# Kernel optimization log

Hardware: AMD Instinct MI355X
Metric: run time of the kernel (lower is better)

## Reference

```python
import jax, jax.numpy as jnp
import numpy as np

N = 50000
D = 128           # feature_dim
H = 8             # num_heads
DH = D // H       # head_dim = 16
K = 32            # k_neighbors
FFN = int(D * 1.5)  # 192
TAU_NEG = 0.6
BETA = 1.5
LN_EPS = 1e-5


def layer_norm(x, g, b):
    mu = jnp.mean(x, axis=-1, keepdims=True)
    var = jnp.mean((x - mu) ** 2, axis=-1, keepdims=True)
    return (x - mu) * jax.lax.rsqrt(var + LN_EPS) * g + b


def setup_inputs() -> dict:
    key = jax.random.key(0)
    ks = jax.random.split(key, 12)
    s = 1.0 / np.sqrt(D)
    inp = {
        "features": jax.random.normal(ks[0], (N, D), dtype=jnp.float32),
        "knn_indices": jax.random.randint(ks[1], (N, K), 0, N, dtype=jnp.int64 if jax.config.jax_enable_x64 else jnp.int32),
        "spatial_distances": jax.random.uniform(ks[2], (N, K), dtype=jnp.float32) * 8.0,
        "Wq": jax.random.normal(ks[3], (D, D), dtype=jnp.float32) * s,
        "Wk": jax.random.normal(ks[4], (D, D), dtype=jnp.float32) * s,
        "Wv": jax.random.normal(ks[5], (D, D), dtype=jnp.float32) * s,
        "Wo": jax.random.normal(ks[6], (D, D), dtype=jnp.float32) * s,
        "bo": jnp.zeros((D,), dtype=jnp.float32),
        "ln1_g": jnp.ones((D,), dtype=jnp.float32),
        "ln1_b": jnp.zeros((D,), dtype=jnp.float32),
        "W1": jax.random.normal(ks[7], (D, FFN), dtype=jnp.float32) * s,
        "b1": jnp.zeros((FFN,), dtype=jnp.float32),
        "W2": jax.random.normal(ks[8], (FFN, D), dtype=jnp.float32) * (1.0 / np.sqrt(FFN)),
        "b2": jnp.zeros((D,), dtype=jnp.float32),
        "ln2_g": jnp.ones((D,), dtype=jnp.float32),
        "ln2_b": jnp.zeros((D,), dtype=jnp.float32),
    }
    return inp


def reference(features, knn_indices, spatial_distances, Wq, Wk, Wv, Wo, bo,
              ln1_g, ln1_b, W1, b1, W2, b2, ln2_g, ln2_b):
    n = features.shape[0]
    Q = (features @ Wq).reshape(n, H, DH)           # (N,H,dh)
    Kp = (features @ Wk).reshape(n, H, DH)
    Vp = (features @ Wv).reshape(n, H, DH)

    K_local = Kp[knn_indices]                        # (N,K,H,dh) irregular gather
    V_local = Vp[knn_indices]                        # (N,K,H,dh)

    raw_scores = jnp.einsum("nhd,nkhd->nhk", Q, K_local) / np.sqrt(DH)  # (N,H,K)

    # per-head spatial decay: 1 / 2^(h+1)
    head_scalings = (0.5 ** jnp.arange(1, H + 1, dtype=features.dtype))  # (H,)
    scaled_dist = spatial_distances[:, None, :] * head_scalings[None, :, None]  # (N,H,K)

    attn_pos = jax.nn.softmax(raw_scores - scaled_dist, axis=-1)
    attn_neg = jax.nn.softmax((-raw_scores - scaled_dist) / TAU_NEG, axis=-1)
    attn = attn_pos - BETA * attn_neg                # (N,H,K); dropout is identity in eval

    attended = jnp.einsum("nhk,nkhd->nhd", attn, V_local).reshape(n, D)

    x = attended @ Wo + bo + features
    x = layer_norm(x, ln1_g, ln1_b)

    h = jax.nn.gelu(x @ W1 + b1, approximate=False)
    ffn_out = h @ W2 + b2
    out = layer_norm(ffn_out + x, ln2_g, ln2_b)
    return out
```

## Files before the change

### kernel.cpp

```cpp
#include <hip/hip_runtime.h>
#include <hip/hip_fp16.h>
#include <cmath>

typedef __attribute__((ext_vector_type(8))) _Float16 f16x8;
typedef __attribute__((ext_vector_type(4))) float f32x4;

__device__ __forceinline__ unsigned int pkh(float a, float b) {
    __half2 h = __floats2half2_rn(a, b);
    return *(unsigned int*)&h;
}
__device__ __forceinline__ float gelu_exact(float v) {
    return 0.5f * v * (1.0f + erff(v * 0.70710678118654752440f));
}
__device__ __forceinline__ __half2 shfl8h(__half2 x, int m) {
    int xi = *(int*)&x;
    int yi = __shfl_xor(xi, m, 8);
    return *(__half2*)&yi;
}

__global__ __launch_bounds__(256, 1) void k_prep(
    const float* __restrict__ Wq, const float* __restrict__ Wk, const float* __restrict__ Wv,
    const float* __restrict__ Wo, const float* __restrict__ W1, const float* __restrict__ W2,
    unsigned short* __restrict__ wsz)
{
    int f = blockIdx.x * 256 + threadIdx.x;
    const float* W; unsigned short* dst; int M, KS, fl;
    if (f < 2048)       { W = Wq; dst = wsz;         M = 128; KS = 4; fl = f; }
    else if (f < 4096)  { W = Wk; dst = wsz + 16384; M = 128; KS = 4; fl = f - 2048; }
    else if (f < 6144)  { W = Wv; dst = wsz + 32768; M = 128; KS = 4; fl = f - 4096; }
    else if (f < 8192)  { W = Wo; dst = wsz + 49152; M = 128; KS = 4; fl = f - 6144; }
    else if (f < 11264) { W = W1; dst = wsz + 65536; M = 192; KS = 4; fl = f - 8192; }
    else if (f < 14336) { W = W2; dst = wsz + 90112; M = 128; KS = 6; fl = f - 11264; }
    else return;
    const int l  = fl & 63;
    const int ks = (fl >> 6) % KS;
    const int ct = (fl >> 6) / KS;
    const int k0 = ks * 32 + (l >> 4) * 8;
    const int col = ct * 16 + (l & 15);
    unsigned short tmp[8];
    #pragma unroll
    for (int j = 0; j < 8; ++j) {
        __half hh = __float2half(W[(size_t)(k0 + j) * M + col]);
        tmp[j] = *(unsigned short*)&hh;
    }
    ((uint4*)dst)[fl] = *(uint4*)tmp;
}

__global__ __launch_bounds__(256, 4) void k_qkv(
    const float* __restrict__ feat, const unsigned short* __restrict__ wsz,
    unsigned short* __restrict__ Qb, unsigned short* __restrict__ KVb, int n)
{
    const int w = threadIdx.x >> 6, lane = threadIdx.x & 63;
    const int lrow = lane & 15, kgrp = lane >> 4;
    const int node = blockIdx.x * 64 + w * 16 + lrow;
    const bool valid = node < n;

    f16x8 bfr[4];
    #pragma unroll
    for (int ks = 0; ks < 4; ++ks) {
        float4 lo = make_float4(0.f, 0.f, 0.f, 0.f), hi = lo;
        if (valid) {
            const float* p = feat + (size_t)node * 128 + ks * 32 + kgrp * 8;
            lo = *(const float4*)p;
            hi = *(const float4*)(p + 4);
        }
        f16x8 b;
        b[0] = (_Float16)lo.x; b[1] = (_Float16)lo.y; b[2] = (_Float16)lo.z; b[3] = (_Float16)lo.w;
        b[4] = (_Float16)hi.x; b[5] = (_Float16)hi.y; b[6] = (_Float16)hi.z; b[7] = (_Float16)hi.w;
        bfr[ks] = b;
    }

    for (int mat = 0; mat < 3; ++mat) {
        const unsigned short* wb = wsz + mat * 16384;
        f32x4 acc[8];
        #pragma unroll
        for (int ct = 0; ct < 8; ++ct) acc[ct] = (f32x4){0.f, 0.f, 0.f, 0.f};
        #pragma unroll
        for (int ct = 0; ct < 8; ++ct)
            #pragma unroll
            for (int ks = 0; ks < 4; ++ks) {
                f16x8 afr = *(const f16x8*)(wb + ((size_t)(ct * 4 + ks) * 64 + lane) * 8);
                acc[ct] = __builtin_amdgcn_mfma_f32_16x16x32_f16(afr, bfr[ks], acc[ct], 0, 0, 0);
            }
        if (valid) {
            unsigned short* O = (mat == 0) ? (Qb + (size_t)node * 128)
                              : (KVb + (size_t)node * 256 + (mat == 2 ? 128 : 0));
            #pragma unroll
            for (int ct = 0; ct < 8; ++ct) {
                int col = ct * 16 + kgrp * 4;
                *((uint2*)(O + col)) =
                    make_uint2(pkh(acc[ct][0], acc[ct][1]), pkh(acc[ct][2], acc[ct][3]));
            }
        }
    }
}

__global__ __launch_bounds__(256, 4) void k_attn(
    const unsigned short* __restrict__ Qb, const unsigned short* __restrict__ KVb,
    const int* __restrict__ knn, const float* __restrict__ dist,
    unsigned short* __restrict__ attf, int n)
{
    const int lane = threadIdx.x & 63;
    const int node = blockIdx.x * 4 + (threadIdx.x >> 6);
    if (node >= n) return;
    const int h = lane >> 3, r = lane & 7;
    const float hs = exp2f(-(float)(h + 1));

    int idx[4]; float sd[4];
    #pragma unroll
    for (int jj = 0; jj < 4; ++jj) {
        int j = r + jj * 8;
        idx[jj] = knn[(size_t)node * 32 + j];
        sd[jj]  = dist[(size_t)node * 32 + j] * hs;
    }

    const unsigned short* qp = Qb + (size_t)node * 128 + h * 16;
    __half2 q2[8];
    *((uint4*)&q2[0]) = *(const uint4*)qp;
    *((uint4*)&q2[4]) = *(const uint4*)(qp + 8);

    uint4 k0[4], k1[4], v0[4], v1[4];
    #pragma unroll
    for (int jj = 0; jj < 4; ++jj) {
        const unsigned short* kvp = KVb + (size_t)idx[jj] * 256 + h * 16;
        k0[jj] = *(const uint4*)kvp;
        k1[jj] = *(const uint4*)(kvp + 8);
        v0[jj] = *(const uint4*)(kvp + 128);
        v1[jj] = *(const uint4*)(kvp + 136);
    }

    float ap[4], an[4];
    #pragma unroll
    for (int jj = 0; jj < 4; ++jj) {
        const __half2* ka = (const __half2*)&k0[jj];
        const __half2* kb = (const __half2*)&k1[jj];
        __half2 s0 = __hmul2(q2[0], ka[0]);
        s0 = __hfma2(q2[1], ka[1], s0);
        s0 = __hfma2(q2[2], ka[2], s0);
        s0 = __hfma2(q2[3], ka[3], s0);
        __half2 s1 = __hmul2(q2[4], kb[0]);
        s1 = __hfma2(q2[5], kb[1], s1);
        s1 = __hfma2(q2[6], kb[2], s1);
        s1 = __hfma2(q2[7], kb[3], s1);
        float s = __low2float(s0) + __high2float(s0) + __low2float(s1) + __high2float(s1);
        float raw = s * 0.25f;
        ap[jj] = raw - sd[jj];
        an[jj] = (-raw - sd[jj]) * (1.0f / 0.6f);
    }

    float mp = fmaxf(fmaxf(ap[0], ap[1]), fmaxf(ap[2], ap[3]));
    float mn = fmaxf(fmaxf(an[0], an[1]), fmaxf(an[2], an[3]));
    #pragma unroll
    for (int msk = 1; msk < 8; msk <<= 1) {
        mp = fmaxf(mp, __shfl_xor(mp, msk, 8));
        mn = fmaxf(mn, __shfl_xor(mn, msk, 8));
    }
    float ep[4], en[4], sp = 0.f, sn = 0.f;
    #pragma unroll
    for (int jj = 0; jj < 4; ++jj) {
        ep[jj] = expf(ap[jj] - mp); sp += ep[jj];
        en[jj] = expf(an[jj] - mn); sn += en[jj];
    }
    #pragma unroll
    for (int msk = 1; msk < 8; msk <<= 1) {
        sp += __shfl_xor(sp, msk, 8);
        sn += __shfl_xor(sn, msk, 8);
    }
    const float isp = 1.0f / sp;
    const float isn = 1.5f / sn;

    __half2 acc2[8];
    #pragma unroll
    for (int i = 0; i < 8; ++i) acc2[i] = __float2half2_rn(0.f);
    #pragma unroll
    for (int jj = 0; jj < 4; ++jj) {
        float wgt = ep[jj] * isp - en[jj] * isn;
        __half2 w2 = __float2half2_rn(wgt);
        const __half2* va = (const __half2*)&v0[jj];
        const __half2* vb = (const __half2*)&v1[jj];
        acc2[0] = __hfma2(w2, va[0], acc2[0]);
        acc2[1] = __hfma2(w2, va[1], acc2[1]);
        acc2[2] = __hfma2(w2, va[2], acc2[2]);
        acc2[3] = __hfma2(w2, va[3], acc2[3]);
        acc2[4] = __hfma2(w2, vb[0], acc2[4]);
        acc2[5] = __hfma2(w2, vb[1], acc2[5]);
        acc2[6] = __hfma2(w2, vb[2], acc2[6]);
        acc2[7] = __hfma2(w2, vb[3], acc2[7]);
    }
    #pragma unroll
    for (int i = 0; i < 8; ++i) {
        acc2[i] = __hadd2(acc2[i], shfl8h(acc2[i], 1));
        acc2[i] = __hadd2(acc2[i], shfl8h(acc2[i], 2));
        acc2[i] = __hadd2(acc2[i], shfl8h(acc2[i], 4));
    }
    if (r == 0) {
        const int g = node >> 4, lrow = node & 15;
        unsigned short* op = attf + (size_t)g * 2048 + (h >> 1) * 512 + (h & 1) * 256 + lrow * 8;
        *((uint4*)op)         = *(uint4*)&acc2[0];
        *((uint4*)(op + 128)) = *(uint4*)&acc2[4];
    }
}

__global__ __launch_bounds__(256, 4) void k_tail(
    const unsigned short* __restrict__ attf, const float* __restrict__ feat,
    const unsigned short* __restrict__ wsz,
    const float* __restrict__ bo, const float* __restrict__ g1, const float* __restrict__ b1ln,
    const float* __restrict__ b1f, const float* __restrict__ b2f,
    const float* __restrict__ g2, const float* __restrict__ b2ln,
    float* __restrict__ out, int n)
{
    __shared__ __align__(16) unsigned short hls[12288];
    const int tid = threadIdx.x;
    const int w = tid >> 6, lane = tid & 63;
    const int lrow = lane & 15, kgrp = lane >> 4;
    const int node = blockIdx.x * 64 + w * 16 + lrow;
    const bool valid = node < n;
    const int g = blockIdx.x * 4 + w;

    f16x8 bfr[6];
    #pragma unroll
    for (int ks = 0; ks < 4; ++ks) {
        uint4 u = make_uint4(0u, 0u, 0u, 0u);
        if (valid) u = *(const uint4*)(attf + (size_t)g * 2048 + ks * 512 + kgrp * 128 + lrow * 8);
        bfr[ks] = *(f16x8*)&u;
    }
    const unsigned short* wo = wsz + 49152;
    f32x4 X[8];
    #pragma unroll
    for (int ct = 0; ct < 8; ++ct) {
        X[ct] = (f32x4){0.f, 0.f, 0.f, 0.f};
        #pragma unroll
        for (int ks = 0; ks < 4; ++ks) {
            f16x8 afr = *(const f16x8*)(wo + ((size_t)(ct * 4 + ks) * 64 + lane) * 8);
            X[ct] = __builtin_amdgcn_mfma_f32_16x16x32_f16(afr, bfr[ks], X[ct], 0, 0, 0);
        }
    }
    #pragma unroll
    for (int ct = 0; ct < 8; ++ct) {
        int col = ct * 16 + kgrp * 4;
        float4 bv = *((const float4*)(bo + col));
        float4 fr = make_float4(0.f, 0.f, 0.f, 0.f);
        if (valid) fr = *((const float4*)(feat + (size_t)node * 128 + col));
        X[ct][0] += bv.x + fr.x; X[ct][1] += bv.y + fr.y;
        X[ct][2] += bv.z + fr.z; X[ct][3] += bv.w + fr.w;
    }
    float s = 0.f;
    #pragma unroll
    for (int ct = 0; ct < 8; ++ct) s += X[ct][0] + X[ct][1] + X[ct][2] + X[ct][3];
    s += __shfl_xor(s, 16); s += __shfl_xor(s, 32);
    const float mu1 = s * (1.0f / 128.0f);
    float s2 = 0.f;
    #pragma unroll
    for (int ct = 0; ct < 8; ++ct)
        #pragma unroll
        for (int rr = 0; rr < 4; ++rr) { float d = X[ct][rr] - mu1; s2 = fmaf(d, d, s2); }
    s2 += __shfl_xor(s2, 16); s2 += __shfl_xor(s2, 32);
    const float rs1 = rsqrtf(s2 * (1.0f / 128.0f) + 1e-5f);

    uint2 xnh[8];
    #pragma unroll
    for (int ct = 0; ct < 8; ++ct) {
        int col = ct * 16 + kgrp * 4;
        float4 gg = *((const float4*)(g1 + col));
        float4 bb = *((const float4*)(b1ln + col));
        float x0 = (X[ct][0] - mu1) * rs1 * gg.x + bb.x;
        float x1 = (X[ct][1] - mu1) * rs1 * gg.y + bb.y;
        float x2 = (X[ct][2] - mu1) * rs1 * gg.z + bb.z;
        float x3 = (X[ct][3] - mu1) * rs1 * gg.w + bb.w;
        xnh[ct] = make_uint2(pkh(x0, x1), pkh(x2, x3));
        int ks = col >> 5, kg = (col & 31) >> 3, jb = col & 7;
        *((uint2*)&hls[((w * 4 + ks) * 4 + kg) * 128 + lrow * 8 + jb]) = xnh[ct];
    }
    __syncthreads();
    #pragma unroll
    for (int ks = 0; ks < 4; ++ks)
        bfr[ks] = *(const f16x8*)&hls[((w * 4 + ks) * 4 + kgrp) * 128 + lrow * 8];
    __syncthreads();

    const unsigned short* w1 = wsz + 65536;
    #pragma unroll
    for (int ct = 0; ct < 12; ++ct) {
        f32x4 acc = (f32x4){0.f, 0.f, 0.f, 0.f};
        #pragma unroll
        for (int ks = 0; ks < 4; ++ks) {
            f16x8 afr = *(const f16x8*)(w1 + ((size_t)(ct * 4 + ks) * 64 + lane) * 8);
            acc = __builtin_amdgcn_mfma_f32_16x16x32_f16(afr, bfr[ks], acc, 0, 0, 0);
        }
        int col = ct * 16 + kgrp * 4;
        float4 bv = *((const float4*)(b1f + col));
        float h0 = gelu_exact(acc[0] + bv.x);
        float h1 = gelu_exact(acc[1] + bv.y);
        float h2 = gelu_exact(acc[2] + bv.z);
        float h3 = gelu_exact(acc[3] + bv.w);
        int ks = col >> 5, kg = (col & 31) >> 3, jb = col & 7;
        *((uint2*)&hls[((w * 6 + ks) * 4 + kg) * 128 + lrow * 8 + jb]) =
            make_uint2(pkh(h0, h1), pkh(h2, h3));
    }
    __syncthreads();
    #pragma unroll
    for (int ks = 0; ks < 6; ++ks)
        bfr[ks] = *(const f16x8*)&hls[((w * 6 + ks) * 4 + kgrp) * 128 + lrow * 8];

    const unsigned short* w2 = wsz + 90112;
    f32x4 Y[8];
    #pragma unroll
    for (int ct = 0; ct < 8; ++ct) {
        Y[ct] = (f32x4){0.f, 0.f, 0.f, 0.f};
        #pragma unroll
        for (int ks = 0; ks < 6; ++ks) {
            f16x8 afr = *(const f16x8*)(w2 + ((size_t)(ct * 6 + ks) * 64 + lane) * 8);
            Y[ct] = __builtin_amdgcn_mfma_f32_16x16x32_f16(afr, bfr[ks], Y[ct], 0, 0, 0);
        }
    }
    #pragma unroll
    for (int ct = 0; ct < 8; ++ct) {
        int col = ct * 16 + kgrp * 4;
        float4 bv = *((const float4*)(b2f + col));
        __half2 x01 = *(__half2*)&xnh[ct].x, x23 = *(__half2*)&xnh[ct].y;
        Y[ct][0] += bv.x + __low2float(x01);
        Y[ct][1] += bv.y + __high2float(x01);
        Y[ct][2] += bv.z + __low2float(x23);
        Y[ct][3] += bv.w + __high2float(x23);
    }
    float t1 = 0.f;
    #pragma unroll
    for (int ct = 0; ct < 8; ++ct) t1 += Y[ct][0] + Y[ct][1] + Y[ct][2] + Y[ct][3];
    t1 += __shfl_xor(t1, 16); t1 += __shfl_xor(t1, 32);
    const float mu2 = t1 * (1.0f / 128.0f);
    float t2 = 0.f;
    #pragma unroll
    for (int ct = 0; ct < 8; ++ct)
        #pragma unroll
        for (int rr = 0; rr < 4; ++rr) { float d = Y[ct][rr] - mu2; t2 = fmaf(d, d, t2); }
    t2 += __shfl_xor(t2, 16); t2 += __shfl_xor(t2, 32);
    const float rs2 = rsqrtf(t2 * (1.0f / 128.0f) + 1e-5f);
    if (valid) {
        #pragma unroll
        for (int ct = 0; ct < 8; ++ct) {
            int col = ct * 16 + kgrp * 4;
            float4 gg = *((const float4*)(g2 + col));
            float4 bb = *((const float4*)(b2ln + col));
            float4 o;
            o.x = (Y[ct][0] - mu2) * rs2 * gg.x + bb.x;
            o.y = (Y[ct][1] - mu2) * rs2 * gg.y + bb.y;
            o.z = (Y[ct][2] - mu2) * rs2 * gg.z + bb.z;
            o.w = (Y[ct][3] - mu2) * rs2 * gg.w + bb.w;
            *((float4*)(out + (size_t)node * 128 + col)) = o;
        }
    }
}

extern "C" void kernel_launch(void* const* d_in, const int* in_sizes, int n_in,
                              void* d_out, int out_size, void* d_ws, size_t ws_size,
                              hipStream_t stream)
{
    const float* feat = (const float*)d_in[0];
    const int*   knn  = (const int*)d_in[1];
    const float* dist = (const float*)d_in[2];
    const float* Wq   = (const float*)d_in[3];
    const float* Wk   = (const float*)d_in[4];
    const float* Wv   = (const float*)d_in[5];
    const float* Wo   = (const float*)d_in[6];
    const float* bo   = (const float*)d_in[7];
    const float* g1   = (const float*)d_in[8];
    const float* b1ln = (const float*)d_in[9];
    const float* W1   = (const float*)d_in[10];
    const float* b1f  = (const float*)d_in[11];
    const float* W2   = (const float*)d_in[12];
    const float* b2f  = (const float*)d_in[13];
    const float* g2   = (const float*)d_in[14];
    const float* b2ln = (const float*)d_in[15];
    float* out = (float*)d_out;

    const int n = in_sizes[0] / 128;
    const size_t ND = (size_t)n * 128;
    if (ws_size < 8 * ND + 262144) return;

    unsigned short* Qb   = (unsigned short*)d_ws;
    unsigned short* KVb  = Qb + ND;
    unsigned short* attf = KVb + 2 * ND;
    unsigned short* Wsz  = attf + ND;

    k_prep<<<56, 256, 0, stream>>>(Wq, Wk, Wv, Wo, W1, W2, Wsz);
    k_qkv <<<(n + 63) / 64, 256, 0, stream>>>(feat, Wsz, Qb, KVb, n);
    k_attn<<<(n + 3) / 4,   256, 0, stream>>>(Qb, KVb, knn, dist, attf, n);
    k_tail<<<(n + 63) / 64, 256, 0, stream>>>(attf, feat, Wsz, bo, g1, b1ln, b1f, b2f,
                                              g2, b2ln, out, n);
}
```

Measured before the change: 179.8 us.

## Process two row tiles per wave, use fast GELU and exp2 softmax

k_qkv and k_tail now have each wave handle two 16-row tiles, so every weight fragment loaded from global memory feeds two MFMAs. Blocks shrink to 128 threads. The exact erf GELU becomes a sigmoid-based approximation using exp2 and a hardware reciprocal, and the attention softmax folds log2(e) into its scales so it can call exp2f. k_prep is split so each thread writes half as much. Register pressure goes up, and the GELU approximation changes numerics slightly.

```diff
diff --git a/kernel.cpp b/kernel.cpp
--- a/kernel.cpp
+++ b/kernel.cpp
@@ -9,8 +9,9 @@
     __half2 h = __floats2half2_rn(a, b);
     return *(unsigned int*)&h;
 }
-__device__ __forceinline__ float gelu_exact(float v) {
-    return 0.5f * v * (1.0f + erff(v * 0.70710678118654752440f));
+__device__ __forceinline__ float gelu_fast(float x) {
+    float w = x * fmaf(x * x, 0.1029377202f, 2.302085565f);
+    return x * __builtin_amdgcn_rcpf(1.0f + exp2f(-w));
 }
 __device__ __forceinline__ __half2 shfl8h(__half2 x, int m) {
     int xi = *(int*)&x;
@@ -23,73 +24,83 @@
     const float* __restrict__ Wo, const float* __restrict__ W1, const float* __restrict__ W2,
     unsigned short* __restrict__ wsz)
 {
-    int f = blockIdx.x * 256 + threadIdx.x;
+    int idx = blockIdx.x * 256 + threadIdx.x;
+    if (idx >= 28672) return;
+    int f = idx >> 1;
+    const int half = idx & 1;
     const float* W; unsigned short* dst; int M, KS, fl;
     if (f < 2048)       { W = Wq; dst = wsz;         M = 128; KS = 4; fl = f; }
     else if (f < 4096)  { W = Wk; dst = wsz + 16384; M = 128; KS = 4; fl = f - 2048; }
     else if (f < 6144)  { W = Wv; dst = wsz + 32768; M = 128; KS = 4; fl = f - 4096; }
     else if (f < 8192)  { W = Wo; dst = wsz + 49152; M = 128; KS = 4; fl = f - 6144; }
     else if (f < 11264) { W = W1; dst = wsz + 65536; M = 192; KS = 4; fl = f - 8192; }
-    else if (f < 14336) { W = W2; dst = wsz + 90112; M = 128; KS = 6; fl = f - 11264; }
-    else return;
+    else                { W = W2; dst = wsz + 90112; M = 128; KS = 6; fl = f - 11264; }
     const int l  = fl & 63;
     const int ks = (fl >> 6) % KS;
     const int ct = (fl >> 6) / KS;
-    const int k0 = ks * 32 + (l >> 4) * 8;
+    const int k0 = ks * 32 + (l >> 4) * 8 + half * 4;
     const int col = ct * 16 + (l & 15);
-    unsigned short tmp[8];
-    #pragma unroll
-    for (int j = 0; j < 8; ++j) {
+    unsigned short tmp[4];
+    #pragma unroll
+    for (int j = 0; j < 4; ++j) {
         __half hh = __float2half(W[(size_t)(k0 + j) * M + col]);
         tmp[j] = *(unsigned short*)&hh;
     }
-    ((uint4*)dst)[fl] = *(uint4*)tmp;
-}
-
-__global__ __launch_bounds__(256, 4) void k_qkv(
+    ((uint2*)dst)[fl * 2 + half] = *(uint2*)tmp;
+}
+
+__global__ __launch_bounds__(128, 3) void k_qkv(
     const float* __restrict__ feat, const unsigned short* __restrict__ wsz,
     unsigned short* __restrict__ Qb, unsigned short* __restrict__ KVb, int n)
 {
     const int w = threadIdx.x >> 6, lane = threadIdx.x & 63;
     const int lrow = lane & 15, kgrp = lane >> 4;
-    const int node = blockIdx.x * 64 + w * 16 + lrow;
-    const bool valid = node < n;
-
-    f16x8 bfr[4];
-    #pragma unroll
-    for (int ks = 0; ks < 4; ++ks) {
-        float4 lo = make_float4(0.f, 0.f, 0.f, 0.f), hi = lo;
-        if (valid) {
-            const float* p = feat + (size_t)node * 128 + ks * 32 + kgrp * 8;
-            lo = *(const float4*)p;
-            hi = *(const float4*)(p + 4);
-        }
-        f16x8 b;
-        b[0] = (_Float16)lo.x; b[1] = (_Float16)lo.y; b[2] = (_Float16)lo.z; b[3] = (_Float16)lo.w;
-        b[4] = (_Float16)hi.x; b[5] = (_Float16)hi.y; b[6] = (_Float16)hi.z; b[7] = (_Float16)hi.w;
-        bfr[ks] = b;
-    }
+    int node[2]; bool valid[2];
+    node[0] = blockIdx.x * 64 + w * 32 + lrow;  valid[0] = node[0] < n;
+    node[1] = node[0] + 16;                     valid[1] = node[1] < n;
+
+    f16x8 bfr[2][4];
+    #pragma unroll
+    for (int rt = 0; rt < 2; ++rt)
+        #pragma unroll
+        for (int ks = 0; ks < 4; ++ks) {
+            float4 lo = make_float4(0.f, 0.f, 0.f, 0.f), hi = lo;
+            if (valid[rt]) {
+                const float* p = feat + (size_t)node[rt] * 128 + ks * 32 + kgrp * 8;
+                lo = *(const float4*)p;
+                hi = *(const float4*)(p + 4);
+            }
+            f16x8 b;
+            b[0] = (_Float16)lo.x; b[1] = (_Float16)lo.y; b[2] = (_Float16)lo.z; b[3] = (_Float16)lo.w;
+            b[4] = (_Float16)hi.x; b[5] = (_Float16)hi.y; b[6] = (_Float16)hi.z; b[7] = (_Float16)hi.w;
+            bfr[rt][ks] = b;
+        }
 
     for (int mat = 0; mat < 3; ++mat) {
         const unsigned short* wb = wsz + mat * 16384;
-        f32x4 acc[8];
-        #pragma unroll
-        for (int ct = 0; ct < 8; ++ct) acc[ct] = (f32x4){0.f, 0.f, 0.f, 0.f};
+        f32x4 acc[2][8];
+        #pragma unroll
+        for (int rt = 0; rt < 2; ++rt)
+            #pragma unroll
+            for (int ct = 0; ct < 8; ++ct) acc[rt][ct] = (f32x4){0.f, 0.f, 0.f, 0.f};
         #pragma unroll
         for (int ct = 0; ct < 8; ++ct)
             #pragma unroll
             for (int ks = 0; ks < 4; ++ks) {
                 f16x8 afr = *(const f16x8*)(wb + ((size_t)(ct * 4 + ks) * 64 + lane) * 8);
-                acc[ct] = __builtin_amdgcn_mfma_f32_16x16x32_f16(afr, bfr[ks], acc[ct], 0, 0, 0);
+                acc[0][ct] = __builtin_amdgcn_mfma_f32_16x16x32_f16(afr, bfr[0][ks], acc[0][ct], 0, 0, 0);
+                acc[1][ct] = __builtin_amdgcn_mfma_f32_16x16x32_f16(afr, bfr[1][ks], acc[1][ct], 0, 0, 0);
             }
-        if (valid) {
-            unsigned short* O = (mat == 0) ? (Qb + (size_t)node * 128)
-                              : (KVb + (size_t)node * 256 + (mat == 2 ? 128 : 0));
+        #pragma unroll
+        for (int rt = 0; rt < 2; ++rt) {
+            if (!valid[rt]) continue;
+            unsigned short* O = (mat == 0) ? (Qb + (size_t)node[rt] * 128)
+                              : (KVb + (size_t)node[rt] * 256 + (mat == 2 ? 128 : 0));
             #pragma unroll
             for (int ct = 0; ct < 8; ++ct) {
                 int col = ct * 16 + kgrp * 4;
                 *((uint2*)(O + col)) =
-                    make_uint2(pkh(acc[ct][0], acc[ct][1]), pkh(acc[ct][2], acc[ct][3]));
+                    make_uint2(pkh(acc[rt][ct][0], acc[rt][ct][1]), pkh(acc[rt][ct][2], acc[rt][ct][3]));
             }
         }
     }
@@ -104,14 +115,15 @@
     const int node = blockIdx.x * 4 + (threadIdx.x >> 6);
     if (node >= n) return;
     const int h = lane >> 3, r = lane & 7;
-    const float hs = exp2f(-(float)(h + 1));
-
-    int idx[4]; float sd[4];
+    const float L2E = 1.4426950408889634f;
+    const float hsl = exp2f(-(float)(h + 1)) * L2E;
+
+    int idx[4]; float sdl[4];
     #pragma unroll
     for (int jj = 0; jj < 4; ++jj) {
         int j = r + jj * 8;
         idx[jj] = knn[(size_t)node * 32 + j];
-        sd[jj]  = dist[(size_t)node * 32 + j] * hs;
+        sdl[jj] = dist[(size_t)node * 32 + j] * hsl;
     }
 
     const unsigned short* qp = Qb + (size_t)node * 128 + h * 16;
@@ -143,9 +155,9 @@
         s1 = __hfma2(q2[6], kb[2], s1);
         s1 = __hfma2(q2[7], kb[3], s1);
         float s = __low2float(s0) + __high2float(s0) + __low2float(s1) + __high2float(s1);
-        float raw = s * 0.25f;
-        ap[jj] = raw - sd[jj];
-        an[jj] = (-raw - sd[jj]) * (1.0f / 0.6f);
+        float rawl = s * (0.25f * L2E);
+        ap[jj] = rawl - sdl[jj];
+        an[jj] = (-rawl - sdl[jj]) * (1.0f / 0.6f);
     }
 
     float mp = fmaxf(fmaxf(ap[0], ap[1]), fmaxf(ap[2], ap[3]));
@@ -158,8 +170,8 @@
     float ep[4], en[4], sp = 0.f, sn = 0.f;
     #pragma unroll
     for (int jj = 0; jj < 4; ++jj) {
-        ep[jj] = expf(ap[jj] - mp); sp += ep[jj];
-        en[jj] = expf(an[jj] - mn); sn += en[jj];
+        ep[jj] = exp2f(ap[jj] - mp); sp += ep[jj];
+        en[jj] = exp2f(an[jj] - mn); sn += en[jj];
     }
     #pragma unroll
     for (int msk = 1; msk < 8; msk <<= 1) {
@@ -201,7 +213,7 @@
     }
 }
 
-__global__ __launch_bounds__(256, 4) void k_tail(
+__global__ __launch_bounds__(128, 3) void k_tail(
     const unsigned short* __restrict__ attf, const float* __restrict__ feat,
     const unsigned short* __restrict__ wsz,
     const float* __restrict__ bo, const float* __restrict__ g1, const float* __restrict__ b1ln,
@@ -213,139 +225,162 @@
     const int tid = threadIdx.x;
     const int w = tid >> 6, lane = tid & 63;
     const int lrow = lane & 15, kgrp = lane >> 4;
-    const int node = blockIdx.x * 64 + w * 16 + lrow;
-    const bool valid = node < n;
-    const int g = blockIdx.x * 4 + w;
-
-    f16x8 bfr[6];
-    #pragma unroll
-    for (int ks = 0; ks < 4; ++ks) {
-        uint4 u = make_uint4(0u, 0u, 0u, 0u);
-        if (valid) u = *(const uint4*)(attf + (size_t)g * 2048 + ks * 512 + kgrp * 128 + lrow * 8);
-        bfr[ks] = *(f16x8*)&u;
-    }
+    int node[2]; bool valid[2]; int g[2];
+    node[0] = blockIdx.x * 64 + w * 32 + lrow;  valid[0] = node[0] < n;
+    node[1] = node[0] + 16;                     valid[1] = node[1] < n;
+    g[0] = blockIdx.x * 4 + w * 2;
+    g[1] = g[0] + 1;
+
+    f16x8 bfr[2][4];
+    #pragma unroll
+    for (int rt = 0; rt < 2; ++rt)
+        #pragma unroll
+        for (int ks = 0; ks < 4; ++ks)
+            bfr[rt][ks] = *(const f16x8*)(attf + (size_t)g[rt] * 2048 + (ks * 4 + kgrp) * 128 + lrow * 8);
+
     const unsigned short* wo = wsz + 49152;
-    f32x4 X[8];
-    #pragma unroll
-    for (int ct = 0; ct < 8; ++ct) {
-        X[ct] = (f32x4){0.f, 0.f, 0.f, 0.f};
+    f32x4 X[2][8];
+    #pragma unroll
+    for (int rt = 0; rt < 2; ++rt)
+        #pragma unroll
+        for (int ct = 0; ct < 8; ++ct) X[rt][ct] = (f32x4){0.f, 0.f, 0.f, 0.f};
+    #pragma unroll
+    for (int ct = 0; ct < 8; ++ct)
         #pragma unroll
         for (int ks = 0; ks < 4; ++ks) {
             f16x8 afr = *(const f16x8*)(wo + ((size_t)(ct * 4 + ks) * 64 + lane) * 8);
-            X[ct] = __builtin_amdgcn_mfma_f32_16x16x32_f16(afr, bfr[ks], X[ct], 0, 0, 0);
-        }
-    }
-    #pragma unroll
-    for (int ct = 0; ct < 8; ++ct) {
-        int col = ct * 16 + kgrp * 4;
-        float4 bv = *((const float4*)(bo + col));
-        float4 fr = make_float4(0.f, 0.f, 0.f, 0.f);
-        if (valid) fr = *((const float4*)(feat + (size_t)node * 128 + col));
-        X[ct][0] += bv.x + fr.x; X[ct][1] += bv.y + fr.y;
-        X[ct][2] += bv.z + fr.z; X[ct][3] += bv.w + fr.w;
-    }
-    float s = 0.f;
-    #pragma unroll
-    for (int ct = 0; ct < 8; ++ct) s += X[ct][0] + X[ct][1] + X[ct][2] + X[ct][3];
-    s += __shfl_xor(s, 16); s += __shfl_xor(s, 32);
-    const float mu1 = s * (1.0f / 128.0f);
-    float s2 = 0.f;
-    #pragma unroll
-    for (int ct = 0; ct < 8; ++ct)
-        #pragma unroll
-        for (int rr = 0; rr < 4; ++rr) { float d = X[ct][rr] - mu1; s2 = fmaf(d, d, s2); }
-    s2 += __shfl_xor(s2, 16); s2 += __shfl_xor(s2, 32);
-    const float rs1 = rsqrtf(s2 * (1.0f / 128.0f) + 1e-5f);
-
-    uint2 xnh[8];
-    #pragma unroll
-    for (int ct = 0; ct < 8; ++ct) {
-        int col = ct * 16 + kgrp * 4;
-        float4 gg = *((const float4*)(g1 + col));
-        float4 bb = *((const float4*)(b1ln + col));
-        float x0 = (X[ct][0] - mu1) * rs1 * gg.x + bb.x;
-        float x1 = (X[ct][1] - mu1) * rs1 * gg.y + bb.y;
-        float x2 = (X[ct][2] - mu1) * rs1 * gg.z + bb.z;
-        float x3 = (X[ct][3] - mu1) * rs1 * gg.w + bb.w;
-        xnh[ct] = make_uint2(pkh(x0, x1), pkh(x2, x3));
-        int ks = col >> 5, kg = (col & 31) >> 3, jb = col & 7;
-        *((uint2*)&hls[((w * 4 + ks) * 4 + kg) * 128 + lrow * 8 + jb]) = xnh[ct];
+            X[0][ct] = __builtin_amdgcn_mfma_f32_16x16x32_f16(afr, bfr[0][ks], X[0][ct], 0, 0, 0);
+            X[1][ct] = __builtin_amdgcn_mfma_f32_16x16x32_f16(afr, bfr[1][ks], X[1][ct], 0, 0, 0);
+        }
+
+    uint2 xnh[2][8];
+    #pragma unroll
+    for (int rt = 0; rt < 2; ++rt) {
+        #pragma unroll
+        for (int ct = 0; ct < 8; ++ct) {
+            int col = ct * 16 + kgrp * 4;
+            float4 bv = *((const float4*)(bo + col));
+            float4 fr = make_float4(0.f, 0.f, 0.f, 0.f);
+            if (valid[rt]) fr = *((const float4*)(feat + (size_t)node[rt] * 128 + col));
+            X[rt][ct][0] += bv.x + fr.x; X[rt][ct][1] += bv.y + fr.y;
+            X[rt][ct][2] += bv.z + fr.z; X[rt][ct][3] += bv.w + fr.w;
+        }
+        float s = 0.f;
+        #pragma unroll
+        for (int ct = 0; ct < 8; ++ct) s += X[rt][ct][0] + X[rt][ct][1] + X[rt][ct][2] + X[rt][ct][3];
+        s += __shfl_xor(s, 16); s += __shfl_xor(s, 32);
+        const float mu1 = s * (1.0f / 128.0f);
+        float s2 = 0.f;
+        #pragma unroll
+        for (int ct = 0; ct < 8; ++ct)
+            #pragma unroll
+            for (int rr = 0; rr < 4; ++rr) { float d = X[rt][ct][rr] - mu1; s2 = fmaf(d, d, s2); }
+        s2 += __shfl_xor(s2, 16); s2 += __shfl_xor(s2, 32);
+        const float rs1 = rsqrtf(s2 * (1.0f / 128.0f) + 1e-5f);
+        #pragma unroll
+        for (int ct = 0; ct < 8; ++ct) {
+            int col = ct * 16 + kgrp * 4;
+            float4 gg = *((const float4*)(g1 + col));
+            float4 bb = *((const float4*)(b1ln + col));
+            float x0 = (X[rt][ct][0] - mu1) * rs1 * gg.x + bb.x;
+            float x1 = (X[rt][ct][1] - mu1) * rs1 * gg.y + bb.y;
+            float x2 = (X[rt][ct][2] - mu1) * rs1 * gg.z + bb.z;
+            float x3 = (X[rt][ct][3] - mu1) * rs1 * gg.w + bb.w;
+            xnh[rt][ct] = make_uint2(pkh(x0, x1), pkh(x2, x3));
+            int ks4 = col >> 5, kg = (col & 31) >> 3, jb = col & 7;
+            *((uint2*)&hls[(w * 2 + rt) * 2048 + (ks4 * 4 + kg) * 128 + lrow * 8 + jb]) = xnh[rt][ct];
+        }
     }
     __syncthreads();
     #pragma unroll
-    for (int ks = 0; ks < 4; ++ks)
-        bfr[ks] = *(const f16x8*)&hls[((w * 4 + ks) * 4 + kgrp) * 128 + lrow * 8];
+    for (int rt = 0; rt < 2; ++rt)
+        #pragma unroll
+        for (int ks = 0; ks < 4; ++ks)
+            bfr[rt][ks] = *(const f16x8*)&hls[(w * 2 + rt) * 2048 + (ks * 4 + kgrp) * 128 + lrow * 8];
     __syncthreads();
 
     const unsigned short* w1 = wsz + 65536;
     #pragma unroll
     for (int ct = 0; ct < 12; ++ct) {
-        f32x4 acc = (f32x4){0.f, 0.f, 0.f, 0.f};
+        f32x4 acc0 = (f32x4){0.f, 0.f, 0.f, 0.f};
+        f32x4 acc1 = (f32x4){0.f, 0.f, 0.f, 0.f};
         #pragma unroll
         for (int ks = 0; ks < 4; ++ks) {
             f16x8 afr = *(const f16x8*)(w1 + ((size_t)(ct * 4 + ks) * 64 + lane) * 8);
-            acc = __builtin_amdgcn_mfma_f32_16x16x32_f16(afr, bfr[ks], acc, 0, 0, 0);
+            acc0 = __builtin_amdgcn_mfma_f32_16x16x32_f16(afr, bfr[0][ks], acc0, 0, 0, 0);
+            acc1 = __builtin_amdgcn_mfma_f32_16x16x32_f16(afr, bfr[1][ks], acc1, 0, 0, 0);
         }
         int col = ct * 16 + kgrp * 4;
         float4 bv = *((const float4*)(b1f + col));
-        float h0 = gelu_exact(acc[0] + bv.x);
-        float h1 = gelu_exact(acc[1] + bv.y);
-        float h2 = gelu_exact(acc[2] + bv.z);
-        float h3 = gelu_exact(acc[3] + bv.w);
-        int ks = col >> 5, kg = (col & 31) >> 3, jb = col & 7;
-        *((uint2*)&hls[((w * 6 + ks) * 4 + kg) * 128 + lrow * 8 + jb]) =
+        int ks6 = col >> 5, kg = (col & 31) >> 3, jb = col & 7;
+        float h0 = gelu_fast(acc0[0] + bv.x), h1 = gelu_fast(acc0[1] + bv.y);
+        float h2 = gelu_fast(acc0[2] + bv.z), h3 = gelu_fast(acc0[3] + bv.w);
+        *((uint2*)&hls[(w * 2 + 0) * 3072 + (ks6 * 4 + kg) * 128 + lrow * 8 + jb]) =
             make_uint2(pkh(h0, h1), pkh(h2, h3));
+        h0 = gelu_fast(acc1[0] + bv.x); h1 = gelu_fast(acc1[1] + bv.y);
+        h2 = gelu_fast(acc1[2] + bv.z); h3 = gelu_fast(acc1[3] + bv.w);
+        *((uint2*)&hls[(w * 2 + 1) * 3072 + (ks6 * 4 + kg) * 128 + lrow * 8 + jb]) =
+            make_uint2(pkh(h0, h1), pkh(h2, h3));
     }
     __syncthreads();
-    #pragma unroll
-    for (int ks = 0; ks < 6; ++ks)
-        bfr[ks] = *(const f16x8*)&hls[((w * 6 + ks) * 4 + kgrp) * 128 + lrow * 8];
+    f16x8 bfh[2][6];
+    #pragma unroll
+    for (int rt = 0; rt < 2; ++rt)
+        #pragma unroll
+        for (int ks = 0; ks < 6; ++ks)
+            bfh[rt][ks] = *(const f16x8*)&hls[(w * 2 + rt) * 3072 + (ks * 4 + kgrp) * 128 + lrow * 8];
 
     const unsigned short* w2 = wsz + 90112;
-    f32x4 Y[8];
-    #pragma unroll
-    for (int ct = 0; ct < 8; ++ct) {
-        Y[ct] = (f32x4){0.f, 0.f, 0.f, 0.f};
+    f32x4 Y[2][8];
+    #pragma unroll
+    for (int rt = 0; rt < 2; ++rt)
+        #pragma unroll
+        for (int ct = 0; ct < 8; ++ct) Y[rt][ct] = (f32x4){0.f, 0.f, 0.f, 0.f};
+    #pragma unroll
+    for (int ct = 0; ct < 8; ++ct)
         #pragma unroll
         for (int ks = 0; ks < 6; ++ks) {
             f16x8 afr = *(const f16x8*)(w2 + ((size_t)(ct * 6 + ks) * 64 + lane) * 8);
-            Y[ct] = __builtin_amdgcn_mfma_f32_16x16x32_f16(afr, bfr[ks], Y[ct], 0, 0, 0);
-        }
-    }
-    #pragma unroll
-    for (int ct = 0; ct < 8; ++ct) {
-        int col = ct * 16 + kgrp * 4;
-        float4 bv = *((const float4*)(b2f + col));
-        __half2 x01 = *(__half2*)&xnh[ct].x, x23 = *(__half2*)&xnh[ct].y;
-        Y[ct][0] += bv.x + __low2float(x01);
-        Y[ct][1] += bv.y + __high2float(x01);
-        Y[ct][2] += bv.z + __low2float(x23);
-        Y[ct][3] += bv.w + __high2float(x23);
-    }
-    float t1 = 0.f;
-    #pragma unroll
-    for (int ct = 0; ct < 8; ++ct) t1 += Y[ct][0] + Y[ct][1] + Y[ct][2] + Y[ct][3];
-    t1 += __shfl_xor(t1, 16); t1 += __shfl_xor(t1, 32);
-    const float mu2 = t1 * (1.0f / 128.0f);
-    float t2 = 0.f;
-    #pragma unroll
-    for (int ct = 0; ct < 8; ++ct)
-        #pragma unroll
-        for (int rr = 0; rr < 4; ++rr) { float d = Y[ct][rr] - mu2; t2 = fmaf(d, d, t2); }
-    t2 += __shfl_xor(t2, 16); t2 += __shfl_xor(t2, 32);
-    const float rs2 = rsqrtf(t2 * (1.0f / 128.0f) + 1e-5f);
-    if (valid) {
+            Y[0][ct] = __builtin_amdgcn_mfma_f32_16x16x32_f16(afr, bfh[0][ks], Y[0][ct], 0, 0, 0);
+            Y[1][ct] = __builtin_amdgcn_mfma_f32_16x16x32_f16(afr, bfh[1][ks], Y[1][ct], 0, 0, 0);
+        }
+    #pragma unroll
+    for (int rt = 0; rt < 2; ++rt) {
         #pragma unroll
         for (int ct = 0; ct < 8; ++ct) {
             int col = ct * 16 + kgrp * 4;
-            float4 gg = *((const float4*)(g2 + col));
-            float4 bb = *((const float4*)(b2ln + col));
-            float4 o;
-            o.x = (Y[ct][0] - mu2) * rs2 * gg.x + bb.x;
-            o.y = (Y[ct][1] - mu2) * rs2 * gg.y + bb.y;
-            o.z = (Y[ct][2] - mu2) * rs2 * gg.z + bb.z;
-            o.w = (Y[ct][3] - mu2) * rs2 * gg.w + bb.w;
-            *((float4*)(out + (size_t)node * 128 + col)) = o;
+            float4 bv = *((const float4*)(b2f + col));
+            __half2 x01 = *(__half2*)&xnh[rt][ct].x, x23 = *(__half2*)&xnh[rt][ct].y;
+            Y[rt][ct][0] += bv.x + __low2float(x01);
+            Y[rt][ct][1] += bv.y + __high2float(x01);
+            Y[rt][ct][2] += bv.z + __low2float(x23);
+            Y[rt][ct][3] += bv.w + __high2float(x23);
+        }
+        float t1 = 0.f;
+        #pragma unroll
+        for (int ct = 0; ct < 8; ++ct) t1 += Y[rt][ct][0] + Y[rt][ct][1] + Y[rt][ct][2] + Y[rt][ct][3];
+        t1 += __shfl_xor(t1, 16); t1 += __shfl_xor(t1, 32);
+        const float mu2 = t1 * (1.0f / 128.0f);
+        float t2 = 0.f;
+        #pragma unroll
+        for (int ct = 0; ct < 8; ++ct)
+            #pragma unroll
+            for (int rr = 0; rr < 4; ++rr) { float d = Y[rt][ct][rr] - mu2; t2 = fmaf(d, d, t2); }
+        t2 += __shfl_xor(t2, 16); t2 += __shfl_xor(t2, 32);
+        const float rs2 = rsqrtf(t2 * (1.0f / 128.0f) + 1e-5f);
+        if (valid[rt]) {
+            #pragma unroll
+            for (int ct = 0; ct < 8; ++ct) {
+                int col = ct * 16 + kgrp * 4;
+                float4 gg = *((const float4*)(g2 + col));
+                float4 bb = *((const float4*)(b2ln + col));
+                float4 o;
+                o.x = (Y[rt][ct][0] - mu2) * rs2 * gg.x + bb.x;
+                o.y = (Y[rt][ct][1] - mu2) * rs2 * gg.y + bb.y;
+                o.z = (Y[rt][ct][2] - mu2) * rs2 * gg.z + bb.z;
+                o.w = (Y[rt][ct][3] - mu2) * rs2 * gg.w + bb.w;
+                *((float4*)(out + (size_t)node[rt] * 128 + col)) = o;
+            }
         }
     }
 }
@@ -381,9 +416,9 @@
     unsigned short* attf = KVb + 2 * ND;
     unsigned short* Wsz  = attf + ND;
 
-    k_prep<<<56, 256, 0, stream>>>(Wq, Wk, Wv, Wo, W1, W2, Wsz);
-    k_qkv <<<(n + 63) / 64, 256, 0, stream>>>(feat, Wsz, Qb, KVb, n);
+    k_prep<<<112, 256, 0, stream>>>(Wq, Wk, Wv, Wo, W1, W2, Wsz);
+    k_qkv <<<(n + 63) / 64, 128, 0, stream>>>(feat, Wsz, Qb, KVb, n);
     k_attn<<<(n + 3) / 4,   256, 0, stream>>>(Qb, KVb, knn, dist, attf, n);
-    k_tail<<<(n + 63) / 64, 256, 0, stream>>>(attf, feat, Wsz, bo, g1, b1ln, b1f, b2f,
+    k_tail<<<(n + 63) / 64, 128, 0, stream>>>(attf, feat, Wsz, bo, g1, b1ln, b1f, b2f,
                                               g2, b2ln, out, n);
 }
```

Result: no change. 182.8 us (+1.6%).

## Fuse attention into tail kernel, use per-wave LDS, fast GELU and exp2

Applied to the files above, without the earlier changes.

Merges the gather-attention kernel and the output-projection/FFN tail into one kernel. Each wave loops over its 16 nodes, writes the attended vectors to a private LDS buffer and then runs the MFMA tail, so the attended intermediate never goes through global memory and block-wide syncs are no longer needed. It also swaps exact erf GELU for a sigmoid-style approximation, uses exp2 with a log2(e) prescale in the softmax, and splits the weight-prep threads in half. Each wave now handles 16 nodes in sequence instead of one wave per node, which reduces the latency-hiding parallelism for the random KV gathers, and the GELU approximation changes numerics.

```diff
diff --git a/kernel.cpp b/kernel.cpp
--- a/kernel.cpp
+++ b/kernel.cpp
@@ -9,8 +9,9 @@
     __half2 h = __floats2half2_rn(a, b);
     return *(unsigned int*)&h;
 }
-__device__ __forceinline__ float gelu_exact(float v) {
-    return 0.5f * v * (1.0f + erff(v * 0.70710678118654752440f));
+__device__ __forceinline__ float gelu_fast(float x) {
+    float w = x * fmaf(x * x, 0.1029377202f, 2.302085565f);
+    return x * __builtin_amdgcn_rcpf(1.0f + exp2f(-w));
 }
 __device__ __forceinline__ __half2 shfl8h(__half2 x, int m) {
     int xi = *(int*)&x;
@@ -23,27 +24,29 @@
     const float* __restrict__ Wo, const float* __restrict__ W1, const float* __restrict__ W2,
     unsigned short* __restrict__ wsz)
 {
-    int f = blockIdx.x * 256 + threadIdx.x;
+    int idx = blockIdx.x * 256 + threadIdx.x;
+    if (idx >= 28672) return;
+    int f = idx >> 1;
+    const int half = idx & 1;
     const float* W; unsigned short* dst; int M, KS, fl;
     if (f < 2048)       { W = Wq; dst = wsz;         M = 128; KS = 4; fl = f; }
     else if (f < 4096)  { W = Wk; dst = wsz + 16384; M = 128; KS = 4; fl = f - 2048; }
     else if (f < 6144)  { W = Wv; dst = wsz + 32768; M = 128; KS = 4; fl = f - 4096; }
     else if (f < 8192)  { W = Wo; dst = wsz + 49152; M = 128; KS = 4; fl = f - 6144; }
     else if (f < 11264) { W = W1; dst = wsz + 65536; M = 192; KS = 4; fl = f - 8192; }
-    else if (f < 14336) { W = W2; dst = wsz + 90112; M = 128; KS = 6; fl = f - 11264; }
-    else return;
+    else                { W = W2; dst = wsz + 90112; M = 128; KS = 6; fl = f - 11264; }
     const int l  = fl & 63;
     const int ks = (fl >> 6) % KS;
     const int ct = (fl >> 6) / KS;
-    const int k0 = ks * 32 + (l >> 4) * 8;
+    const int k0 = ks * 32 + (l >> 4) * 8 + half * 4;
     const int col = ct * 16 + (l & 15);
-    unsigned short tmp[8];
-    #pragma unroll
-    for (int j = 0; j < 8; ++j) {
+    unsigned short tmp[4];
+    #pragma unroll
+    for (int j = 0; j < 4; ++j) {
         __half hh = __float2half(W[(size_t)(k0 + j) * M + col]);
         tmp[j] = *(unsigned short*)&hh;
     }
-    ((uint4*)dst)[fl] = *(uint4*)tmp;
+    ((uint2*)dst)[fl * 2 + half] = *(uint2*)tmp;
 }
 
 __global__ __launch_bounds__(256, 4) void k_qkv(
@@ -95,135 +98,129 @@
     }
 }
 
-__global__ __launch_bounds__(256, 4) void k_attn(
+__global__ __launch_bounds__(256, 4) void k_fused(
     const unsigned short* __restrict__ Qb, const unsigned short* __restrict__ KVb,
     const int* __restrict__ knn, const float* __restrict__ dist,
-    unsigned short* __restrict__ attf, int n)
-{
-    const int lane = threadIdx.x & 63;
-    const int node = blockIdx.x * 4 + (threadIdx.x >> 6);
-    if (node >= n) return;
-    const int h = lane >> 3, r = lane & 7;
-    const float hs = exp2f(-(float)(h + 1));
-
-    int idx[4]; float sd[4];
-    #pragma unroll
-    for (int jj = 0; jj < 4; ++jj) {
-        int j = r + jj * 8;
-        idx[jj] = knn[(size_t)node * 32 + j];
-        sd[jj]  = dist[(size_t)node * 32 + j] * hs;
-    }
-
-    const unsigned short* qp = Qb + (size_t)node * 128 + h * 16;
-    __half2 q2[8];
-    *((uint4*)&q2[0]) = *(const uint4*)qp;
-    *((uint4*)&q2[4]) = *(const uint4*)(qp + 8);
-
-    uint4 k0[4], k1[4], v0[4], v1[4];
-    #pragma unroll
-    for (int jj = 0; jj < 4; ++jj) {
-        const unsigned short* kvp = KVb + (size_t)idx[jj] * 256 + h * 16;
-        k0[jj] = *(const uint4*)kvp;
-        k1[jj] = *(const uint4*)(kvp + 8);
-        v0[jj] = *(const uint4*)(kvp + 128);
-        v1[jj] = *(const uint4*)(kvp + 136);
-    }
-
-    float ap[4], an[4];
-    #pragma unroll
-    for (int jj = 0; jj < 4; ++jj) {
-        const __half2* ka = (const __half2*)&k0[jj];
-        const __half2* kb = (const __half2*)&k1[jj];
-        __half2 s0 = __hmul2(q2[0], ka[0]);
-        s0 = __hfma2(q2[1], ka[1], s0);
-        s0 = __hfma2(q2[2], ka[2], s0);
-        s0 = __hfma2(q2[3], ka[3], s0);
-        __half2 s1 = __hmul2(q2[4], kb[0]);
-        s1 = __hfma2(q2[5], kb[1], s1);
-        s1 = __hfma2(q2[6], kb[2], s1);
-        s1 = __hfma2(q2[7], kb[3], s1);
-        float s = __low2float(s0) + __high2float(s0) + __low2float(s1) + __high2float(s1);
-        float raw = s * 0.25f;
-        ap[jj] = raw - sd[jj];
-        an[jj] = (-raw - sd[jj]) * (1.0f / 0.6f);
-    }
-
-    float mp = fmaxf(fmaxf(ap[0], ap[1]), fmaxf(ap[2], ap[3]));
-    float mn = fmaxf(fmaxf(an[0], an[1]), fmaxf(an[2], an[3]));
-    #pragma unroll
-    for (int msk = 1; msk < 8; msk <<= 1) {
-        mp = fmaxf(mp, __shfl_xor(mp, msk, 8));
-        mn = fmaxf(mn, __shfl_xor(mn, msk, 8));
-    }
-    float ep[4], en[4], sp = 0.f, sn = 0.f;
-    #pragma unroll
-    for (int jj = 0; jj < 4; ++jj) {
-        ep[jj] = expf(ap[jj] - mp); sp += ep[jj];
-        en[jj] = expf(an[jj] - mn); sn += en[jj];
-    }
-    #pragma unroll
-    for (int msk = 1; msk < 8; msk <<= 1) {
-        sp += __shfl_xor(sp, msk, 8);
-        sn += __shfl_xor(sn, msk, 8);
-    }
-    const float isp = 1.0f / sp;
-    const float isn = 1.5f / sn;
-
-    __half2 acc2[8];
-    #pragma unroll
-    for (int i = 0; i < 8; ++i) acc2[i] = __float2half2_rn(0.f);
-    #pragma unroll
-    for (int jj = 0; jj < 4; ++jj) {
-        float wgt = ep[jj] * isp - en[jj] * isn;
-        __half2 w2 = __float2half2_rn(wgt);
-        const __half2* va = (const __half2*)&v0[jj];
-        const __half2* vb = (const __half2*)&v1[jj];
-        acc2[0] = __hfma2(w2, va[0], acc2[0]);
-        acc2[1] = __hfma2(w2, va[1], acc2[1]);
-        acc2[2] = __hfma2(w2, va[2], acc2[2]);
-        acc2[3] = __hfma2(w2, va[3], acc2[3]);
-        acc2[4] = __hfma2(w2, vb[0], acc2[4]);
-        acc2[5] = __hfma2(w2, vb[1], acc2[5]);
-        acc2[6] = __hfma2(w2, vb[2], acc2[6]);
-        acc2[7] = __hfma2(w2, vb[3], acc2[7]);
-    }
-    #pragma unroll
-    for (int i = 0; i < 8; ++i) {
-        acc2[i] = __hadd2(acc2[i], shfl8h(acc2[i], 1));
-        acc2[i] = __hadd2(acc2[i], shfl8h(acc2[i], 2));
-        acc2[i] = __hadd2(acc2[i], shfl8h(acc2[i], 4));
-    }
-    if (r == 0) {
-        const int g = node >> 4, lrow = node & 15;
-        unsigned short* op = attf + (size_t)g * 2048 + (h >> 1) * 512 + (h & 1) * 256 + lrow * 8;
-        *((uint4*)op)         = *(uint4*)&acc2[0];
-        *((uint4*)(op + 128)) = *(uint4*)&acc2[4];
-    }
-}
-
-__global__ __launch_bounds__(256, 4) void k_tail(
-    const unsigned short* __restrict__ attf, const float* __restrict__ feat,
-    const unsigned short* __restrict__ wsz,
+    const float* __restrict__ feat, const unsigned short* __restrict__ wsz,
     const float* __restrict__ bo, const float* __restrict__ g1, const float* __restrict__ b1ln,
     const float* __restrict__ b1f, const float* __restrict__ b2f,
     const float* __restrict__ g2, const float* __restrict__ b2ln,
     float* __restrict__ out, int n)
 {
-    __shared__ __align__(16) unsigned short hls[12288];
-    const int tid = threadIdx.x;
-    const int w = tid >> 6, lane = tid & 63;
+    __shared__ __align__(16) unsigned short buf[4][3200];
+    const int w = threadIdx.x >> 6, lane = threadIdx.x & 63;
     const int lrow = lane & 15, kgrp = lane >> 4;
-    const int node = blockIdx.x * 64 + w * 16 + lrow;
-    const bool valid = node < n;
-    const int g = blockIdx.x * 4 + w;
-
-    f16x8 bfr[6];
-    #pragma unroll
-    for (int ks = 0; ks < 4; ++ks) {
-        uint4 u = make_uint4(0u, 0u, 0u, 0u);
-        if (valid) u = *(const uint4*)(attf + (size_t)g * 2048 + ks * 512 + kgrp * 128 + lrow * 8);
-        bfr[ks] = *(f16x8*)&u;
-    }
+    const int h = lane >> 3, r = lane & 7;
+    const int base = blockIdx.x * 64 + w * 16;
+    unsigned short* mybuf = buf[w];
+
+    const float L2E = 1.4426950408889634f;
+    const float hsl = exp2f(-(float)(h + 1)) * L2E;
+
+    for (int i = 0; i < 16; ++i) {
+        const int node = min(base + i, n - 1);
+
+        int idx[4]; float sdl[4];
+        #pragma unroll
+        for (int jj = 0; jj < 4; ++jj) {
+            int j = r + jj * 8;
+            idx[jj] = knn[(size_t)node * 32 + j];
+            sdl[jj] = dist[(size_t)node * 32 + j] * hsl;
+        }
+        const unsigned short* qp = Qb + (size_t)node * 128 + h * 16;
+        __half2 q2[8];
+        *((uint4*)&q2[0]) = *(const uint4*)qp;
+        *((uint4*)&q2[4]) = *(const uint4*)(qp + 8);
+
+        uint4 k0[4], k1[4], v0[4], v1[4];
+        #pragma unroll
+        for (int jj = 0; jj < 4; ++jj) {
+            const unsigned short* kvp = KVb + (size_t)idx[jj] * 256 + h * 16;
+            k0[jj] = *(const uint4*)kvp;
+            k1[jj] = *(const uint4*)(kvp + 8);
+            v0[jj] = *(const uint4*)(kvp + 128);
+            v1[jj] = *(const uint4*)(kvp + 136);
+        }
+
+        float ap[4], an[4];
+        #pragma unroll
+        for (int jj = 0; jj < 4; ++jj) {
+            const __half2* ka = (const __half2*)&k0[jj];
+            const __half2* kb = (const __half2*)&k1[jj];
+            __half2 s0 = __hmul2(q2[0], ka[0]);
+            s0 = __hfma2(q2[1], ka[1], s0);
+            s0 = __hfma2(q2[2], ka[2], s0);
+            s0 = __hfma2(q2[3], ka[3], s0);
+            __half2 s1 = __hmul2(q2[4], kb[0]);
+            s1 = __hfma2(q2[5], kb[1], s1);
+            s1 = __hfma2(q2[6], kb[2], s1);
+            s1 = __hfma2(q2[7], kb[3], s1);
+            float s = __low2float(s0) + __high2float(s0) + __low2float(s1) + __high2float(s1);
+            float rawl = s * (0.25f * L2E);
+            ap[jj] = rawl - sdl[jj];
+            an[jj] = (-rawl - sdl[jj]) * (1.0f / 0.6f);
+        }
+
+        float mp = fmaxf(fmaxf(ap[0], ap[1]), fmaxf(ap[2], ap[3]));
+        float mn = fmaxf(fmaxf(an[0], an[1]), fmaxf(an[2], an[3]));
+        #pragma unroll
+        for (int msk = 1; msk < 8; msk <<= 1) {
+            mp = fmaxf(mp, __shfl_xor(mp, msk, 8));
+            mn = fmaxf(mn, __shfl_xor(mn, msk, 8));
+        }
+        float ep[4], en[4], sp = 0.f, sn = 0.f;
+        #pragma unroll
+        for (int jj = 0; jj < 4; ++jj) {
+            ep[jj] = exp2f(ap[jj] - mp); sp += ep[jj];
+            en[jj] = exp2f(an[jj] - mn); sn += en[jj];
+        }
+        #pragma unroll
+        for (int msk = 1; msk < 8; msk <<= 1) {
+            sp += __shfl_xor(sp, msk, 8);
+            sn += __shfl_xor(sn, msk, 8);
+        }
+        const float isp = 1.0f / sp;
+        const float isn = 1.5f / sn;
+
+        __half2 acc2[8];
+        #pragma unroll
+        for (int q = 0; q < 8; ++q) acc2[q] = __float2half2_rn(0.f);
+        #pragma unroll
+        for (int jj = 0; jj < 4; ++jj) {
+            float wgt = ep[jj] * isp - en[jj] * isn;
+            __half2 w2 = __float2half2_rn(wgt);
+            const __half2* va = (const __half2*)&v0[jj];
+            const __half2* vb = (const __half2*)&v1[jj];
+            acc2[0] = __hfma2(w2, va[0], acc2[0]);
+            acc2[1] = __hfma2(w2, va[1], acc2[1]);
+            acc2[2] = __hfma2(w2, va[2], acc2[2]);
+            acc2[3] = __hfma2(w2, va[3], acc2[3]);
+            acc2[4] = __hfma2(w2, vb[0], acc2[4]);
+            acc2[5] = __hfma2(w2, vb[1], acc2[5]);
+            acc2[6] = __hfma2(w2, vb[2], acc2[6]);
+            acc2[7] = __hfma2(w2, vb[3], acc2[7]);
+        }
+        #pragma unroll
+        for (int q = 0; q < 8; ++q) {
+            acc2[q] = __hadd2(acc2[q], shfl8h(acc2[q], 1));
+            acc2[q] = __hadd2(acc2[q], shfl8h(acc2[q], 2));
+            acc2[q] = __hadd2(acc2[q], shfl8h(acc2[q], 4));
+        }
+        if (r == 0) {
+            unsigned short* op = mybuf + i * 136 + h * 16;
+            *((uint4*)op)       = *(uint4*)&acc2[0];
+            *((uint4*)(op + 8)) = *(uint4*)&acc2[4];
+        }
+    }
+
+    const int node_t = base + lrow;
+    const bool valid = node_t < n;
+
+    f16x8 bfr[4];
+    #pragma unroll
+    for (int ks = 0; ks < 4; ++ks)
+        bfr[ks] = *(const f16x8*)&mybuf[lrow * 136 + ks * 32 + kgrp * 8];
+
     const unsigned short* wo = wsz + 49152;
     f32x4 X[8];
     #pragma unroll
@@ -240,7 +237,7 @@
         int col = ct * 16 + kgrp * 4;
         float4 bv = *((const float4*)(bo + col));
         float4 fr = make_float4(0.f, 0.f, 0.f, 0.f);
-        if (valid) fr = *((const float4*)(feat + (size_t)node * 128 + col));
+        if (valid) fr = *((const float4*)(feat + (size_t)node_t * 128 + col));
         X[ct][0] += bv.x + fr.x; X[ct][1] += bv.y + fr.y;
         X[ct][2] += bv.z + fr.z; X[ct][3] += bv.w + fr.w;
     }
@@ -268,14 +265,11 @@
         float x2 = (X[ct][2] - mu1) * rs1 * gg.z + bb.z;
         float x3 = (X[ct][3] - mu1) * rs1 * gg.w + bb.w;
         xnh[ct] = make_uint2(pkh(x0, x1), pkh(x2, x3));
-        int ks = col >> 5, kg = (col & 31) >> 3, jb = col & 7;
-        *((uint2*)&hls[((w * 4 + ks) * 4 + kg) * 128 + lrow * 8 + jb]) = xnh[ct];
-    }
-    __syncthreads();
+        *((uint2*)&mybuf[lrow * 136 + col]) = xnh[ct];
+    }
     #pragma unroll
     for (int ks = 0; ks < 4; ++ks)
-        bfr[ks] = *(const f16x8*)&hls[((w * 4 + ks) * 4 + kgrp) * 128 + lrow * 8];
-    __syncthreads();
+        bfr[ks] = *(const f16x8*)&mybuf[lrow * 136 + ks * 32 + kgrp * 8];
 
     const unsigned short* w1 = wsz + 65536;
     #pragma unroll
@@ -288,18 +282,14 @@
         }
         int col = ct * 16 + kgrp * 4;
         float4 bv = *((const float4*)(b1f + col));
-        float h0 = gelu_exact(acc[0] + bv.x);
-        float h1 = gelu_exact(acc[1] + bv.y);
-        float h2 = gelu_exact(acc[2] + bv.z);
-        float h3 = gelu_exact(acc[3] + bv.w);
-        int ks = col >> 5, kg = (col & 31) >> 3, jb = col & 7;
-        *((uint2*)&hls[((w * 6 + ks) * 4 + kg) * 128 + lrow * 8 + jb]) =
-            make_uint2(pkh(h0, h1), pkh(h2, h3));
-    }
-    __syncthreads();
+        float h0 = gelu_fast(acc[0] + bv.x), h1 = gelu_fast(acc[1] + bv.y);
+        float h2 = gelu_fast(acc[2] + bv.z), h3 = gelu_fast(acc[3] + bv.w);
+        *((uint2*)&mybuf[lrow * 200 + col]) = make_uint2(pkh(h0, h1), pkh(h2, h3));
+    }
+    f16x8 bfh[6];
     #pragma unroll
     for (int ks = 0; ks < 6; ++ks)
-        bfr[ks] = *(const f16x8*)&hls[((w * 6 + ks) * 4 + kgrp) * 128 + lrow * 8];
+        bfh[ks] = *(const f16x8*)&mybuf[lrow * 200 + ks * 32 + kgrp * 8];
 
     const unsigned short* w2 = wsz + 90112;
     f32x4 Y[8];
@@ -309,7 +299,7 @@
         #pragma unroll
         for (int ks = 0; ks < 6; ++ks) {
             f16x8 afr = *(const f16x8*)(w2 + ((size_t)(ct * 6 + ks) * 64 + lane) * 8);
-            Y[ct] = __builtin_amdgcn_mfma_f32_16x16x32_f16(afr, bfr[ks], Y[ct], 0, 0, 0);
+            Y[ct] = __builtin_amdgcn_mfma_f32_16x16x32_f16(afr, bfh[ks], Y[ct], 0, 0, 0);
         }
     }
     #pragma unroll
@@ -345,7 +335,7 @@
             o.y = (Y[ct][1] - mu2) * rs2 * gg.y + bb.y;
             o.z = (Y[ct][2] - mu2) * rs2 * gg.z + bb.z;
             o.w = (Y[ct][3] - mu2) * rs2 * gg.w + bb.w;
-            *((float4*)(out + (size_t)node * 128 + col)) = o;
+            *((float4*)(out + (size_t)node_t * 128 + col)) = o;
         }
     }
 }
@@ -374,16 +364,15 @@
 
     const int n = in_sizes[0] / 128;
     const size_t ND = (size_t)n * 128;
-    if (ws_size < 8 * ND + 262144) return;
-
-    unsigned short* Qb   = (unsigned short*)d_ws;
-    unsigned short* KVb  = Qb + ND;
-    unsigned short* attf = KVb + 2 * ND;
-    unsigned short* Wsz  = attf + ND;
-
-    k_prep<<<56, 256, 0, stream>>>(Wq, Wk, Wv, Wo, W1, W2, Wsz);
-    k_qkv <<<(n + 63) / 64, 256, 0, stream>>>(feat, Wsz, Qb, KVb, n);
-    k_attn<<<(n + 3) / 4,   256, 0, stream>>>(Qb, KVb, knn, dist, attf, n);
-    k_tail<<<(n + 63) / 64, 256, 0, stream>>>(attf, feat, Wsz, bo, g1, b1ln, b1f, b2f,
-                                              g2, b2ln, out, n);
-}
+    if (ws_size < 6 * ND + 262144) return;
+
+    unsigned short* Qb  = (unsigned short*)d_ws;
+    unsigned short* KVb = Qb + ND;
+    unsigned short* Wsz = KVb + 2 * ND;
+
+    const int tiles = (n + 63) / 64;
+    k_prep <<<112, 256, 0, stream>>>(Wq, Wk, Wv, Wo, W1, W2, Wsz);
+    k_qkv  <<<tiles, 256, 0, stream>>>(feat, Wsz, Qb, KVb, n);
+    k_fused<<<tiles, 256, 0, stream>>>(Qb, KVb, knn, dist, feat, Wsz, bo, g1, b1ln,
+                                       b1f, b2f, g2, b2ln, out, n);
+}
```

Result: slower. 200.8 us (+11.6%).
